# Optimization experiments

Hardware: AMD Instinct MI355X
Metric: run time of the kernel (lower is better)

The kernel has to match this reference:

```python
import jax, jax.numpy as jnp
from jax import lax
import numpy as np

R = 500          # Resampling: temporal segment width
H = 100          # fixed signal height from the reshape in forward
EPS = 1e-5       # BatchNorm2d default eps
FLAT = 6 * 31 * 32


def _cbrp(x, w, b, g, be, m, v):
    """Conv(5x5, pad 2) + inference BatchNorm + ReLU + MaxPool 2x2."""
    x = lax.conv_general_dilated(x, w, (1, 1), ((2, 2), (2, 2)),
                                 dimension_numbers=('NCHW', 'OIHW', 'NCHW'))
    x = x + b[None, :, None, None]
    inv = g * lax.rsqrt(v + EPS)
    x = x * inv[None, :, None, None] + (be - m * inv)[None, :, None, None]
    x = jax.nn.relu(x)
    return lax.reduce_window(x, -jnp.inf, lax.max, (1, 1, 2, 2), (1, 1, 2, 2), 'VALID')


def setup_inputs() -> dict:
    key = jax.random.key(0)
    ks = jax.random.split(key, 16)
    d = {}
    d['x'] = jax.random.normal(ks[0], (16, 1, 100, 4000), dtype=jnp.float32)
    chans = [(1, 16), (16, 32), (32, 64), (64, 32)]
    for i, (ci, co) in enumerate(chans, start=1):
        fan_in = ci * 25
        d[f'w{i}'] = jax.random.normal(ks[i], (co, ci, 5, 5), dtype=jnp.float32) * np.float32((2.0 / fan_in) ** 0.5)
        d[f'b{i}'] = jnp.zeros((co,), jnp.float32)
        d[f'g{i}'] = jnp.ones((co,), jnp.float32)
        d[f'be{i}'] = jnp.zeros((co,), jnp.float32)
        d[f'm{i}'] = jnp.zeros((co,), jnp.float32)
        d[f'v{i}'] = jnp.ones((co,), jnp.float32)
    d['fw1'] = jax.random.normal(ks[5], (32, FLAT), dtype=jnp.float32) * np.float32(FLAT ** -0.5)
    d['fb1'] = jnp.zeros((32,), jnp.float32)
    d['fw2'] = jax.random.normal(ks[6], (2, 32), dtype=jnp.float32) * np.float32(32 ** -0.5)
    d['fb2'] = jnp.zeros((2,), jnp.float32)
    return d


def reference(x, w1, b1, g1, be1, m1, v1,
              w2, b2, g2, be2, m2, v2,
              w3, b3, g3, be3, m3, v3,
              w4, b4, g4, be4, m4, v4,
              fw1, fb1, fw2, fb2):
    B = x.shape[0]
    L = x.shape[-1] // R  # number of temporal segments per sample
    # (B,1,100,L*R) -> (B*L,1,100,R): batch all segments into one conv call
    xs = x[:, 0].reshape(B, H, L, R).transpose(0, 2, 1, 3).reshape(B * L, 1, H, R)
    h = _cbrp(xs, w1, b1, g1, be1, m1, v1)   # (BL,16,50,250)
    h = _cbrp(h, w2, b2, g2, be2, m2, v2)    # (BL,32,25,125)
    h = _cbrp(h, w3, b3, g3, be3, m3, v3)    # (BL,64,12,62)
    h = _cbrp(h, w4, b4, g4, be4, m4, v4)    # (BL,32,6,31)
    h = h.reshape(B * L, FLAT)
    h = h @ fw1.T + fb1
    h = h @ fw2.T + fb2                      # (BL,2)
    return h.reshape(B, L, 2).mean(axis=1)   # average segment votes per sample
```

## Files before the change

### kernel.cpp

```cpp
#include <hip/hip_runtime.h>
#include <hip/hip_bf16.h>

#define EPSB 1e-5f

typedef short s16x8 __attribute__((ext_vector_type(8)));
typedef float f32x16 __attribute__((ext_vector_type(16)));

#define P1_OFF   0
#define P2_OFF   57507840
#define P3_OFF   89817088
#define L4_OFF   107642880
#define H1_OFF   110690304
#define WT2_OFF  110706688
#define WT3_OFF  110732288
#define WT4_OFF  110834688
#define SS2_OFF  110937088
#define SS3_OFF  110937344
#define SS4_OFF  110937856

__device__ __forceinline__ unsigned short bf16bits(float f) {
    __hip_bfloat16 h = __float2bfloat16(f);
    union { __hip_bfloat16 h; unsigned short u; } cv; cv.h = h; return cv.u;
}


template<int HP, int WP, int C, int IH, int IW>
__device__ __forceinline__ void pad_body(__hip_bfloat16* __restrict__ buf, int idx)
{
    if (idx >= 128 * HP * WP) return;
    const int rc = idx % (HP * WP);
    const int row = rc / WP, col = rc % WP;
    const bool pad = (row < 2) | (row >= 2 + IH) | (col < 2) | (col >= 2 + IW);
    if (!pad) return;
    int4* p = reinterpret_cast<int4*>(buf + (size_t)idx * C);
    #pragma unroll
    for (int i = 0; i < C * 2 / 16; ++i) p[i] = int4{0, 0, 0, 0};
}

__device__ __forceinline__ void wtrans_body(const float* __restrict__ src,
                                            __hip_bfloat16* __restrict__ dst,
                                            int CO, int CI, int idx)
{
    if (idx >= CO * CI * 25) return;
    const int co  = idx / (CI * 25);
    const int rem = idx % (CI * 25);
    const int ci  = rem / 25;
    const int tap = rem % 25;
    dst[((size_t)tap * CO + co) * CI + ci] = __float2bfloat16(src[idx]);
}

__device__ __forceinline__ void scsh_body(const float* __restrict__ b,
                                          const float* __restrict__ g,
                                          const float* __restrict__ be,
                                          const float* __restrict__ m,
                                          const float* __restrict__ v,
                                          float* __restrict__ out, int CO, int i)
{
    if (i < CO) {
        const float sc = g[i] * rsqrtf(v[i] + EPSB);
        out[i]      = sc;
        out[CO + i] = fmaf(b[i] - m[i], sc, be[i]);
    }
}

__global__ __launch_bounds__(256)
void prep_kernel(__hip_bfloat16* p1, __hip_bfloat16* p2, __hip_bfloat16* p3,
                 const float* w2, __hip_bfloat16* wt2,
                 const float* w3, __hip_bfloat16* wt3,
                 const float* w4, __hip_bfloat16* wt4,
                 const float* b2, const float* g2, const float* be2,
                 const float* m2, const float* v2, float* ss2,
                 const float* b3, const float* g3, const float* be3,
                 const float* m3, const float* v3, float* ss3,
                 const float* b4, const float* g4, const float* be4,
                 const float* m4, const float* v4, float* ss4)
{
    const int bid = blockIdx.x;
    const int tid = threadIdx.x;
    if      (bid < 7020) pad_body<54, 260, 16, 50, 250>(p1, bid * 256 + tid);
    else if (bid < 8992) pad_body<29, 136, 32, 25, 125>(p2, (bid - 7020) * 256 + tid);
    else if (bid < 9536) pad_body<16,  68, 64, 12,  62>(p3, (bid - 8992) * 256 + tid);
    else if (bid < 9586) wtrans_body(w2, wt2, 32, 16, (bid - 9536) * 256 + tid);
    else if (bid < 9786) wtrans_body(w3, wt3, 64, 32, (bid - 9586) * 256 + tid);
    else if (bid < 9986) wtrans_body(w4, wt4, 32, 64, (bid - 9786) * 256 + tid);
    else {
        const int which = bid - 9986;
        if      (which == 0) scsh_body(b2, g2, be2, m2, v2, ss2, 32, tid);
        else if (which == 1) scsh_body(b3, g3, be3, m3, v3, ss3, 64, tid);
        else                 scsh_body(b4, g4, be4, m4, v4, ss4, 32, tid);
    }
}

__global__ __launch_bounds__(256, 1)
void conv1_kernel(const float* __restrict__ x,
                  const float* __restrict__ wgt,
                  const float* __restrict__ bias,
                  const float* __restrict__ g,
                  const float* __restrict__ be,
                  const float* __restrict__ m,
                  const float* __restrict__ v,
                  __hip_bfloat16* __restrict__ p1)
{
    const int n   = blockIdx.y;
    const int idx = blockIdx.x * 256 + threadIdx.x;
    if (idx >= 50 * 250) return;
    const int ph = idx / 250, pw = idx % 250;

    const int b = n >> 3, l = n & 7;
    const float* ib = x + (size_t)b * 400000 + l * 500;

    const int h0  = 2 * ph - 2;
    const int w0c = 2 * pw - 2;
    float win[6][6];
    #pragma unroll
    for (int r = 0; r < 6; ++r) {
        const int hh = h0 + r;
        const bool vr = (hh >= 0) & (hh < 100);
        #pragma unroll
        for (int c = 0; c < 6; ++c) {
            const int ww = w0c + c;
            const bool ok = vr & (ww >= 0) & (ww < 500);
            win[r][c] = ok ? ib[hh * 4000 + ww] : 0.0f;
        }
    }
    #pragma unroll
    for (int r = 0; r < 6; ++r)
        #pragma unroll
        for (int c = 0; c < 6; ++c)
            asm volatile("" : "+v"(win[r][c]));

    int packed[8];
    #pragma unroll
    for (int cp = 0; cp < 8; ++cp) {
        unsigned short h2[2];
        #pragma unroll
        for (int sub = 0; sub < 2; ++sub) {
            const int co = 2 * cp + sub;
            float a0 = 0.f, a1 = 0.f, a2 = 0.f, a3 = 0.f;
            #pragma unroll
            for (int kh = 0; kh < 5; ++kh) {
                #pragma unroll
                for (int kw = 0; kw < 5; ++kw) {
                    const float w = wgt[co * 25 + kh * 5 + kw];
                    a0 = fmaf(w, win[kh  ][kw  ], a0);
                    a1 = fmaf(w, win[kh  ][kw+1], a1);
                    a2 = fmaf(w, win[kh+1][kw  ], a2);
                    a3 = fmaf(w, win[kh+1][kw+1], a3);
                }
            }
            const float sc = g[co] * rsqrtf(v[co] + EPSB);
            const float sh = fmaf(bias[co] - m[co], sc, be[co]);
            #define RA(a) fmaxf(fmaf((a), sc, sh), 0.0f)
            h2[sub] = bf16bits(fmaxf(fmaxf(RA(a0), RA(a1)), fmaxf(RA(a2), RA(a3))));
            #undef RA
        }
        packed[cp] = h2[0] | (h2[1] << 16);
    }

    int4* dst = reinterpret_cast<int4*>(
        p1 + (size_t)n * (54 * 260 * 16) + ((2 + ph) * 260 + (2 + pw)) * 16);
    dst[0] = int4{packed[0], packed[1], packed[2], packed[3]};
    dst[1] = int4{packed[4], packed[5], packed[6], packed[7]};
}

template<int CI, int CO, int HINP, int WINP, int HOUTP, int WOUTP,
         int PH, int PW, int NT, int NCOT, int RPW, bool NCHW_OUT>
__global__ __launch_bounds__(256)
void conv_mfma(const __hip_bfloat16* __restrict__ pin,
               const __hip_bfloat16* __restrict__ wq,
               const float* __restrict__ scsh,
               void* __restrict__ pout)
{
    constexpr int R = (PH + RPW - 1) / RPW;
    constexpr int NROW = 2 * RPW + 4;
    const int lane = threadIdx.x & 63;
    int t = blockIdx.x * 4 + (threadIdx.x >> 6);
    const int cot = t % NCOT; t /= NCOT;
    const int wt  = t % NT;   t /= NT;
    const int r   = t % R;    t /= R;
    const int n   = t;
    if (n >= 128) return;

    const int lw = lane & 31, loct = lane >> 5;
    const int co0 = cot * 32;
    const int w0  = wt * 32;

    const __hip_bfloat16* bbase = pin + (size_t)n * (HINP * WINP * CI)
                                + (w0 + lw) * CI + loct * 8;
    const __hip_bfloat16* abase = wq + (co0 + lw) * CI + loct * 8;

    f32x16 acc[2 * RPW];
    #pragma unroll
    for (int q = 0; q < 2 * RPW; ++q) acc[q] = (f32x16){};

    #pragma unroll
    for (int kw = 0; kw < 5; ++kw) {
        #pragma unroll
        for (int s = 0; s < CI / 16; ++s) {
            s16x8 bfr[NROW];
            #pragma unroll
            for (int j = 0; j < NROW; ++j) {
                const int row = (2 * RPW * r + j < HINP) ? (2 * RPW * r + j) : (HINP - 1);
                bfr[j] = *reinterpret_cast<const s16x8*>(bbase + (row * WINP + kw) * CI + s * 16);
            }
            #pragma unroll
            for (int kh = 0; kh < 5; ++kh) {
                const s16x8 a = *reinterpret_cast<const s16x8*>(
                    abase + (size_t)((kh * 5 + kw) * CO) * CI + s * 16);
                #pragma unroll
                for (int q = 0; q < 2 * RPW; ++q)
                    acc[q] = __builtin_amdgcn_mfma_f32_32x32x16_bf16(a, bfr[kh + q], acc[q], 0, 0, 0);
            }
        }
    }

    const int pw = wt * 16 + (lw >> 1);
    const bool act = ((lane & 1) == 0) && (pw < PW);
    #pragma unroll
    for (int p = 0; p < RPW; ++p) {
        const int pr = RPW * r + p;
        const bool rok = (pr < PH);
        #pragma unroll
        for (int reg = 0; reg < 16; ++reg) {
            const int co = co0 + (reg & 3) + 8 * (reg >> 2) + 4 * loct;
            const float sc = scsh[co], sh = scsh[CO + co];
            const float v0 = fmaxf(fmaf(acc[2 * p    ][reg], sc, sh), 0.0f);
            const float v1 = fmaxf(fmaf(acc[2 * p + 1][reg], sc, sh), 0.0f);
            float vm = fmaxf(v0, v1);
            vm = fmaxf(vm, __shfl_xor(vm, 1, 64));
            if (act && rok) {
                if (NCHW_OUT) {
                    ((float*)pout)[(((size_t)n * CO + co) * PH + pr) * PW + pw] = vm;
                } else {
                    ((__hip_bfloat16*)pout)[(size_t)n * (HOUTP * WOUTP * CO)
                        + ((2 + pr) * WOUTP + (2 + pw)) * CO + co] = __float2bfloat16(vm);
                }
            }
        }
    }
}

__global__ __launch_bounds__(64)
void fc1_kernel(const float* __restrict__ h,
                const float* __restrict__ fw1,
                const float* __restrict__ fb1,
                float* __restrict__ h1)
{
    const int n = blockIdx.x;
    const int j = blockIdx.y;
    const int lane = threadIdx.x;
    const float* hp = h   + (size_t)n * 5952;
    const float* wp = fw1 + (size_t)j * 5952;
    float s = 0.0f;
    for (int k = lane; k < 5952; k += 64) s = fmaf(hp[k], wp[k], s);
    #pragma unroll
    for (int off = 32; off > 0; off >>= 1) s += __shfl_down(s, off, 64);
    if (lane == 0) h1[n * 32 + j] = s + fb1[j];
}

__global__ __launch_bounds__(64)
void fc2_mean_kernel(const float* __restrict__ h1,
                     const float* __restrict__ fw2,
                     const float* __restrict__ fb2,
                     float* __restrict__ out)
{
    const int t = threadIdx.x;
    if (t >= 32) return;
    const int b = t >> 1, c = t & 1;
    float s = 0.0f;
    for (int l = 0; l < 8; ++l) {
        const float* hp = h1 + (size_t)(b * 8 + l) * 32;
        #pragma unroll
        for (int j = 0; j < 32; ++j) s = fmaf(hp[j], fw2[c * 32 + j], s);
    }
    out[t] = fmaf(s, 0.125f, fb2[c]);
}

extern "C" void kernel_launch(void* const* d_in, const int* in_sizes, int n_in,
                              void* d_out, int out_size, void* d_ws, size_t ws_size,
                              hipStream_t stream)
{
    const float* x   = (const float*)d_in[0];
    const float* w1  = (const float*)d_in[1];
    const float* b1  = (const float*)d_in[2];
    const float* g1  = (const float*)d_in[3];
    const float* be1 = (const float*)d_in[4];
    const float* m1  = (const float*)d_in[5];
    const float* v1  = (const float*)d_in[6];
    const float* w2  = (const float*)d_in[7];
    const float* b2  = (const float*)d_in[8];
    const float* g2  = (const float*)d_in[9];
    const float* be2 = (const float*)d_in[10];
    const float* m2  = (const float*)d_in[11];
    const float* v2  = (const float*)d_in[12];
    const float* w3  = (const float*)d_in[13];
    const float* b3  = (const float*)d_in[14];
    const float* g3  = (const float*)d_in[15];
    const float* be3 = (const float*)d_in[16];
    const float* m3  = (const float*)d_in[17];
    const float* v3  = (const float*)d_in[18];
    const float* w4  = (const float*)d_in[19];
    const float* b4  = (const float*)d_in[20];
    const float* g4  = (const float*)d_in[21];
    const float* be4 = (const float*)d_in[22];
    const float* m4  = (const float*)d_in[23];
    const float* v4  = (const float*)d_in[24];
    const float* fw1 = (const float*)d_in[25];
    const float* fb1 = (const float*)d_in[26];
    const float* fw2 = (const float*)d_in[27];
    const float* fb2 = (const float*)d_in[28];

    char* ws = (char*)d_ws;
    __hip_bfloat16* p1  = (__hip_bfloat16*)(ws + P1_OFF);
    __hip_bfloat16* p2  = (__hip_bfloat16*)(ws + P2_OFF);
    __hip_bfloat16* p3  = (__hip_bfloat16*)(ws + P3_OFF);
    float*          l4  = (float*)(ws + L4_OFF);
    float*          h1  = (float*)(ws + H1_OFF);
    __hip_bfloat16* wt2 = (__hip_bfloat16*)(ws + WT2_OFF);
    __hip_bfloat16* wt3 = (__hip_bfloat16*)(ws + WT3_OFF);
    __hip_bfloat16* wt4 = (__hip_bfloat16*)(ws + WT4_OFF);
    float*          ss2 = (float*)(ws + SS2_OFF);
    float*          ss3 = (float*)(ws + SS3_OFF);
    float*          ss4 = (float*)(ws + SS4_OFF);

    prep_kernel<<<dim3(9989), 256, 0, stream>>>(
        p1, p2, p3, w2, wt2, w3, wt3, w4, wt4,
        b2, g2, be2, m2, v2, ss2,
        b3, g3, be3, m3, v3, ss3,
        b4, g4, be4, m4, v4, ss4);

    conv1_kernel<<<dim3(49, 128), 256, 0, stream>>>(x, w1, b1, g1, be1, m1, v1, p1);

    conv_mfma<16, 32, 54, 260, 29, 136, 25, 125, 8, 1, 2, false>
        <<<dim3(128 * 13 * 8 / 4), 256, 0, stream>>>(p1, wt2, ss2, p2);
    conv_mfma<32, 64, 29, 136, 16, 68, 12, 62, 4, 2, 2, false>
        <<<dim3(128 * 6 * 4 * 2 / 4), 256, 0, stream>>>(p2, wt3, ss3, p3);
    conv_mfma<64, 32, 16, 68, 0, 0, 6, 31, 2, 1, 1, true>
        <<<dim3(128 * 6 * 2 / 4), 256, 0, stream>>>(p3, wt4, ss4, l4);

    fc1_kernel<<<dim3(128, 32), 64, 0, stream>>>(l4, fw1, fb1, h1);
    fc2_mean_kernel<<<1, 64, 0, stream>>>(h1, fw2, fb2, (float*)d_out);
}
```

Before: 456.6 us.

## Relax conv1 launch bounds, split conv1 launches, swizzle conv_mfma block order

Drops the one-block-per-CU launch bound and the asm register pinning in conv1, and computes all 16 channel outputs before packing them to bf16. This gives the compiler freedom over register allocation and may allow higher occupancy. conv1 now runs as four launches over 32 segments each instead of one. conv_mfma reorders block indices with an XCD-style stride-8 swizzle, aiming at better cache locality across chiplets. The swizzle assumes the grid size is divisible by 8, and the extra launches add launch overhead.

New measurement: 466.7 us. +2.2%, slower.

```diff
diff --git a/kernel.cpp b/kernel.cpp
--- a/kernel.cpp
+++ b/kernel.cpp
@@ -91,7 +91,7 @@
     }
 }
 
-__global__ __launch_bounds__(256, 1)
+__global__ __launch_bounds__(256)
 void conv1_kernel(const float* __restrict__ x,
                   const float* __restrict__ wgt,
                   const float* __restrict__ bias,
@@ -99,9 +99,10 @@
                   const float* __restrict__ be,
                   const float* __restrict__ m,
                   const float* __restrict__ v,
-                  __hip_bfloat16* __restrict__ p1)
-{
-    const int n   = blockIdx.y;
+                  __hip_bfloat16* __restrict__ p1,
+                  int n0)
+{
+    const int n   = blockIdx.y + n0;
     const int idx = blockIdx.x * 256 + threadIdx.x;
     if (idx >= 50 * 250) return;
     const int ph = idx / 250, pw = idx % 250;
@@ -123,44 +124,42 @@
             win[r][c] = ok ? ib[hh * 4000 + ww] : 0.0f;
         }
     }
-    #pragma unroll
-    for (int r = 0; r < 6; ++r)
-        #pragma unroll
-        for (int c = 0; c < 6; ++c)
-            asm volatile("" : "+v"(win[r][c]));
-
-    int packed[8];
-    #pragma unroll
-    for (int cp = 0; cp < 8; ++cp) {
-        unsigned short h2[2];
-        #pragma unroll
-        for (int sub = 0; sub < 2; ++sub) {
-            const int co = 2 * cp + sub;
-            float a0 = 0.f, a1 = 0.f, a2 = 0.f, a3 = 0.f;
+
+    float o[16];
+    #pragma unroll
+    for (int co = 0; co < 16; ++co) {
+        float a0 = 0.f, a1 = 0.f, a2 = 0.f, a3 = 0.f;
+        #pragma unroll
+        for (int kh = 0; kh < 5; ++kh) {
             #pragma unroll
-            for (int kh = 0; kh < 5; ++kh) {
-                #pragma unroll
-                for (int kw = 0; kw < 5; ++kw) {
-                    const float w = wgt[co * 25 + kh * 5 + kw];
-                    a0 = fmaf(w, win[kh  ][kw  ], a0);
-                    a1 = fmaf(w, win[kh  ][kw+1], a1);
-                    a2 = fmaf(w, win[kh+1][kw  ], a2);
-                    a3 = fmaf(w, win[kh+1][kw+1], a3);
-                }
+            for (int kw = 0; kw < 5; ++kw) {
+                const float w = wgt[co * 25 + kh * 5 + kw];
+                a0 = fmaf(w, win[kh  ][kw  ], a0);
+                a1 = fmaf(w, win[kh  ][kw+1], a1);
+                a2 = fmaf(w, win[kh+1][kw  ], a2);
+                a3 = fmaf(w, win[kh+1][kw+1], a3);
             }
-            const float sc = g[co] * rsqrtf(v[co] + EPSB);
-            const float sh = fmaf(bias[co] - m[co], sc, be[co]);
-            #define RA(a) fmaxf(fmaf((a), sc, sh), 0.0f)
-            h2[sub] = bf16bits(fmaxf(fmaxf(RA(a0), RA(a1)), fmaxf(RA(a2), RA(a3))));
-            #undef RA
         }
-        packed[cp] = h2[0] | (h2[1] << 16);
-    }
-
+        const float sc = g[co] * rsqrtf(v[co] + EPSB);
+        const float sh = fmaf(bias[co] - m[co], sc, be[co]);
+        #define RA(a) fmaxf(fmaf((a), sc, sh), 0.0f)
+        o[co] = fmaxf(fmaxf(RA(a0), RA(a1)), fmaxf(RA(a2), RA(a3)));
+        #undef RA
+    }
+
+    int4 v0, v1;
+    v0.x = bf16bits(o[0])  | (bf16bits(o[1])  << 16);
+    v0.y = bf16bits(o[2])  | (bf16bits(o[3])  << 16);
+    v0.z = bf16bits(o[4])  | (bf16bits(o[5])  << 16);
+    v0.w = bf16bits(o[6])  | (bf16bits(o[7])  << 16);
+    v1.x = bf16bits(o[8])  | (bf16bits(o[9])  << 16);
+    v1.y = bf16bits(o[10]) | (bf16bits(o[11]) << 16);
+    v1.z = bf16bits(o[12]) | (bf16bits(o[13]) << 16);
+    v1.w = bf16bits(o[14]) | (bf16bits(o[15]) << 16);
     int4* dst = reinterpret_cast<int4*>(
         p1 + (size_t)n * (54 * 260 * 16) + ((2 + ph) * 260 + (2 + pw)) * 16);
-    dst[0] = int4{packed[0], packed[1], packed[2], packed[3]};
-    dst[1] = int4{packed[4], packed[5], packed[6], packed[7]};
+    dst[0] = v0;
+    dst[1] = v1;
 }
 
 template<int CI, int CO, int HINP, int WINP, int HOUTP, int WOUTP,
@@ -174,7 +173,9 @@
     constexpr int R = (PH + RPW - 1) / RPW;
     constexpr int NROW = 2 * RPW + 4;
     const int lane = threadIdx.x & 63;
-    int t = blockIdx.x * 4 + (threadIdx.x >> 6);
+    const int nbk  = gridDim.x;
+    const int swz  = (blockIdx.x & 7) * (nbk >> 3) + (blockIdx.x >> 3);
+    int t = swz * 4 + (threadIdx.x >> 6);
     const int cot = t % NCOT; t /= NCOT;
     const int wt  = t % NT;   t /= NT;
     const int r   = t % R;    t /= R;
@@ -329,7 +330,9 @@
         b3, g3, be3, m3, v3, ss3,
         b4, g4, be4, m4, v4, ss4);
 
-    conv1_kernel<<<dim3(49, 128), 256, 0, stream>>>(x, w1, b1, g1, be1, m1, v1, p1);
+    for (int c = 0; c < 4; ++c)
+        conv1_kernel<<<dim3(49, 32), 256, 0, stream>>>(
+            x, w1, b1, g1, be1, m1, v1, p1, c * 32);
 
     conv_mfma<16, 32, 54, 260, 29, 136, 25, 125, 8, 1, 2, false>
         <<<dim3(128 * 13 * 8 / 4), 256, 0, stream>>>(p1, wt2, ss2, p2);
```

## Stage conv1 input rows in LDS, swizzle MFMA block order, raise rows per wave

Applied to the files above, without the earlier changes.

conv1 now assigns one pooled output row per block and cooperatively loads the six needed input rows into shared memory, then each thread reads its 6x6 window from LDS. This replaces the per-thread strided global gathers and their redundant overlap. Conv1 is split into four launches of 32 segments each. The MFMA conv kernels get a block-index swizzle and double the rows-per-wave (RPW), which cuts the grid size and raises per-wave reuse at the cost of more accumulator registers. The extra launches and the larger register footprint could lower occupancy or add overhead.

New measurement: 470.8 us. 1.03x slower.

```diff
diff --git a/kernel.cpp b/kernel.cpp
--- a/kernel.cpp
+++ b/kernel.cpp
@@ -91,7 +91,7 @@
     }
 }
 
-__global__ __launch_bounds__(256, 1)
+__global__ __launch_bounds__(256)
 void conv1_kernel(const float* __restrict__ x,
                   const float* __restrict__ wgt,
                   const float* __restrict__ bias,
@@ -99,40 +99,40 @@
                   const float* __restrict__ be,
                   const float* __restrict__ m,
                   const float* __restrict__ v,
-                  __hip_bfloat16* __restrict__ p1)
-{
-    const int n   = blockIdx.y;
-    const int idx = blockIdx.x * 256 + threadIdx.x;
-    if (idx >= 50 * 250) return;
-    const int ph = idx / 250, pw = idx % 250;
+                  __hip_bfloat16* __restrict__ p1,
+                  int n0)
+{
+    __shared__ float smem[6 * 504];
+    const int n   = blockIdx.y + n0;
+    const int ph  = blockIdx.x;
+    const int tid = threadIdx.x;
 
     const int b = n >> 3, l = n & 7;
     const float* ib = x + (size_t)b * 400000 + l * 500;
-
-    const int h0  = 2 * ph - 2;
-    const int w0c = 2 * pw - 2;
+    const int h0 = 2 * ph - 2;
+
+    for (int i = tid; i < 6 * 504; i += 256) {
+        const int rr = i / 504, cc = i % 504;
+        const int hh = h0 + rr, ww = cc - 2;
+        const bool ok = (hh >= 0) & (hh < 100) & (ww >= 0) & (ww < 500);
+        smem[i] = ok ? ib[hh * 4000 + ww] : 0.0f;
+    }
+    __syncthreads();
+
+    if (tid >= 250) return;
+    const int pw = tid;
+
     float win[6][6];
     #pragma unroll
-    for (int r = 0; r < 6; ++r) {
-        const int hh = h0 + r;
-        const bool vr = (hh >= 0) & (hh < 100);
-        #pragma unroll
-        for (int c = 0; c < 6; ++c) {
-            const int ww = w0c + c;
-            const bool ok = vr & (ww >= 0) & (ww < 500);
-            win[r][c] = ok ? ib[hh * 4000 + ww] : 0.0f;
-        }
-    }
-    #pragma unroll
     for (int r = 0; r < 6; ++r)
         #pragma unroll
         for (int c = 0; c < 6; ++c)
-            asm volatile("" : "+v"(win[r][c]));
+            win[r][c] = smem[r * 504 + 2 * pw + c];
 
     int packed[8];
     #pragma unroll
     for (int cp = 0; cp < 8; ++cp) {
-        unsigned short h2[2];
+        unsigned short hb[2];
         #pragma unroll
         for (int sub = 0; sub < 2; ++sub) {
             const int co = 2 * cp + sub;
@@ -151,10 +151,10 @@
             const float sc = g[co] * rsqrtf(v[co] + EPSB);
             const float sh = fmaf(bias[co] - m[co], sc, be[co]);
             #define RA(a) fmaxf(fmaf((a), sc, sh), 0.0f)
-            h2[sub] = bf16bits(fmaxf(fmaxf(RA(a0), RA(a1)), fmaxf(RA(a2), RA(a3))));
+            hb[sub] = bf16bits(fmaxf(fmaxf(RA(a0), RA(a1)), fmaxf(RA(a2), RA(a3))));
             #undef RA
         }
-        packed[cp] = h2[0] | (h2[1] << 16);
+        packed[cp] = hb[0] | (hb[1] << 16);
     }
 
     int4* dst = reinterpret_cast<int4*>(
@@ -174,7 +174,9 @@
     constexpr int R = (PH + RPW - 1) / RPW;
     constexpr int NROW = 2 * RPW + 4;
     const int lane = threadIdx.x & 63;
-    int t = blockIdx.x * 4 + (threadIdx.x >> 6);
+    const int nbk  = gridDim.x;
+    const int swz  = (blockIdx.x & 7) * (nbk >> 3) + (blockIdx.x >> 3);
+    int t = swz * 4 + (threadIdx.x >> 6);
     const int cot = t % NCOT; t /= NCOT;
     const int wt  = t % NT;   t /= NT;
     const int r   = t % R;    t /= R;
@@ -329,14 +331,16 @@
         b3, g3, be3, m3, v3, ss3,
         b4, g4, be4, m4, v4, ss4);
 
-    conv1_kernel<<<dim3(49, 128), 256, 0, stream>>>(x, w1, b1, g1, be1, m1, v1, p1);
-
-    conv_mfma<16, 32, 54, 260, 29, 136, 25, 125, 8, 1, 2, false>
-        <<<dim3(128 * 13 * 8 / 4), 256, 0, stream>>>(p1, wt2, ss2, p2);
-    conv_mfma<32, 64, 29, 136, 16, 68, 12, 62, 4, 2, 2, false>
-        <<<dim3(128 * 6 * 4 * 2 / 4), 256, 0, stream>>>(p2, wt3, ss3, p3);
-    conv_mfma<64, 32, 16, 68, 0, 0, 6, 31, 2, 1, 1, true>
-        <<<dim3(128 * 6 * 2 / 4), 256, 0, stream>>>(p3, wt4, ss4, l4);
+    for (int c = 0; c < 4; ++c)
+        conv1_kernel<<<dim3(50, 32), 256, 0, stream>>>(
+            x, w1, b1, g1, be1, m1, v1, p1, c * 32);
+
+    conv_mfma<16, 32, 54, 260, 29, 136, 25, 125, 8, 1, 4, false>
+        <<<dim3(128 * 7 * 8 / 4), 256, 0, stream>>>(p1, wt2, ss2, p2);
+    conv_mfma<32, 64, 29, 136, 16, 68, 12, 62, 4, 2, 4, false>
+        <<<dim3(128 * 3 * 4 * 2 / 4), 256, 0, stream>>>(p2, wt3, ss3, p3);
+    conv_mfma<64, 32, 16, 68, 0, 0, 6, 31, 2, 1, 2, true>
+        <<<dim3(128 * 3 * 2 / 4), 256, 0, stream>>>(p3, wt4, ss4, l4);
 
     fc1_kernel<<<dim3(128, 32), 64, 0, stream>>>(l4, fw1, fb1, h1);
     fc2_mean_kernel<<<1, 64, 0, stream>>>(h1, fw2, fb2, (float*)d_out);
```
